# Optimization experiments

Measured on AMD Instinct MI355X. Metric: run time of the kernel, lower is better.

## Reference

```python
import jax, jax.numpy as jnp
import numpy as np

SCALE = 0.08838834764831845  # 1/sqrt(128)
NUM_HEADS = 32
NUM_KV_HEADS = 8
HEAD_DIM = 128
BLOCK_SIZE = 16
NUM_BLOCKS = 4096
MAX_BLOCKS_PER_SEQ = 128
BATCH = 32
MAX_CTX = MAX_BLOCKS_PER_SEQ * BLOCK_SIZE  # 2048


def setup_inputs() -> dict:
    key = jax.random.key(0)
    ks = jax.random.split(key, 8)
    D = NUM_KV_HEADS * HEAD_DIM
    q = jax.random.normal(ks[0], (BATCH, NUM_HEADS, HEAD_DIM), dtype=jnp.float32)
    k = jax.random.normal(ks[1], (BATCH, NUM_KV_HEADS, HEAD_DIM), dtype=jnp.float32)
    v = jax.random.normal(ks[2], (BATCH, NUM_KV_HEADS, HEAD_DIM), dtype=jnp.float32)
    k_cache = jax.random.normal(ks[3], (NUM_BLOCKS, BLOCK_SIZE, D), dtype=jnp.float32)
    v_cache = jax.random.normal(ks[4], (NUM_BLOCKS, BLOCK_SIZE, D), dtype=jnp.float32)
    # one unique slot per decoding request (deterministic scatter)
    slot_mapping = jnp.arange(BATCH, dtype=jnp.int32)
    block_tables = jax.random.randint(ks[5], (BATCH, MAX_BLOCKS_PER_SEQ), 0, NUM_BLOCKS, dtype=jnp.int32)
    context_lens = jnp.maximum(
        jax.random.randint(ks[6], (BATCH,), 0, MAX_CTX, dtype=jnp.int32), 1)
    return {"q": q, "k": k, "v": v, "k_cache": k_cache, "v_cache": v_cache,
            "slot_mapping": slot_mapping, "block_tables": block_tables,
            "context_lens": context_lens}


def reference(q, k, v, k_cache, v_cache, slot_mapping, block_tables, context_lens):
    B, H, Dh = q.shape
    KVH = k.shape[1]
    num_blocks, block_size, D = k_cache.shape
    n_rep = H // KVH

    # --- store_kvcache: scatter new K/V tokens into the paged cache ---
    # flat slot index = block_idx * block_size + slot_idx; slot == -1 dropped
    kc = k_cache.reshape(num_blocks * block_size, D)
    vc = v_cache.reshape(num_blocks * block_size, D)
    kc = kc.at[slot_mapping].set(k.reshape(B, D), mode="drop")
    vc = vc.at[slot_mapping].set(v.reshape(B, D), mode="drop")
    kc = kc.reshape(num_blocks, block_size, D)
    vc = vc.reshape(num_blocks, block_size, D)

    # --- decode-phase paged attention ---
    # gather per-request KV via block tables: [B, S, KVH, Dh]
    k_seq = kc[block_tables].reshape(B, -1, KVH, Dh)
    v_seq = vc[block_tables].reshape(B, -1, KVH, Dh)
    S = k_seq.shape[1]

    # GQA: group query heads over kv heads
    qg = q.reshape(B, KVH, n_rep, Dh)
    scores = jnp.einsum("bkgd,bskd->bkgs", qg, k_seq) * SCALE  # [B,KVH,G,S]
    valid = jnp.arange(S, dtype=jnp.int32)[None, :] < context_lens[:, None]  # [B,S]
    scores = jnp.where(valid[:, None, None, :], scores, jnp.float32(-1e30))
    p = jax.nn.softmax(scores, axis=-1)
    out = jnp.einsum("bkgs,bskd->bkgd", p, v_seq)
    return out.reshape(B, H, Dh)
```

## Files before the change

### kernel.cpp

```cpp
#include <hip/hip_runtime.h>
#include <math.h>

#define NH      32
#define KVH     8
#define GRP     4
#define DH      128
#define BS      16
#define D_TOT   1024
#define MBPS    128
#define MAX_CTX 2048
#define SCALE_F 0.08838834764831845f
#define PSTRIDE 136

__global__ void store_kv_kernel(const float* __restrict__ k,
                                const float* __restrict__ v,
                                float* __restrict__ kc,
                                float* __restrict__ vc,
                                const int* __restrict__ slot_mapping) {
    int b = blockIdx.x;
    int t = threadIdx.x;
    int s = slot_mapping[b];
    if (s < 0) return;
    const float4* k4 = (const float4*)(k + (size_t)b * D_TOT);
    const float4* v4 = (const float4*)(v + (size_t)b * D_TOT);
    float4* kc4 = (float4*)(kc + (size_t)s * D_TOT);
    float4* vc4 = (float4*)(vc + (size_t)s * D_TOT);
    kc4[t] = k4[t];
    vc4[t] = v4[t];
}

__global__ __launch_bounds__(256, 6) void attn_partial_kernel(
    const float* __restrict__ q,
    const float* __restrict__ kc,
    const float* __restrict__ vc,
    const int* __restrict__ block_tables,
    const int* __restrict__ ctx_lens,
    float* __restrict__ ws,
    int split_tok, int nsplit)
{
    const int kvh   = blockIdx.x;
    const int b     = blockIdx.y;
    const int split = blockIdx.z;
    const int ctx   = ctx_lens[b];
    const int start = split * split_tok;
    if (start >= ctx) return;
    const int end = min(ctx, start + split_tok);

    const int wave = threadIdx.x >> 6;
    const int lane = threadIdx.x & 63;
    const int h    = kvh * GRP + wave;
    const int tsub = lane >> 4;
    const int dseg = lane & 15;

    const float* qh = q + ((size_t)b * NH + h) * DH;
    const float4 qa = *(const float4*)(qh + dseg * 8);
    const float4 qb = *(const float4*)(qh + dseg * 8 + 4);

    const int* bt = block_tables + b * MBPS;

    float m = -INFINITY;
    float l = 0.f;
    float acc[8];
    #pragma unroll
    for (int j = 0; j < 8; ++j) acc[j] = 0.f;

    const int cb0 = start >> 4;
    const int cb1 = (end + 15) >> 4;

    for (int cb = cb0; cb < cb1; ++cb) {
        const int blk = bt[cb];
        const float* kbase = kc + (size_t)blk * BS * D_TOT + kvh * DH;
        const float* vbase = vc + (size_t)blk * BS * D_TOT + kvh * DH;
        const int tbase = cb << 4;

        #pragma unroll 2
        for (int ps = 0; ps < 4; ++ps) {
            const int tok  = tbase + ps * 4 + tsub;
            const int rofs = (ps * 4 + tsub) * D_TOT + dseg * 8;
            float4 ka = *(const float4*)(kbase + rofs);
            float4 kb = *(const float4*)(kbase + rofs + 4);
            float4 va = *(const float4*)(vbase + rofs);
            float4 vb = *(const float4*)(vbase + rofs + 4);

            float s = qa.x*ka.x + qa.y*ka.y + qa.z*ka.z + qa.w*ka.w
                    + qb.x*kb.x + qb.y*kb.y + qb.z*kb.z + qb.w*kb.w;
            s += __shfl_xor(s, 1);
            s += __shfl_xor(s, 2);
            s += __shfl_xor(s, 4);
            s += __shfl_xor(s, 8);
            s *= SCALE_F;
            if (tok >= end) s = -INFINITY;

            float pm = fmaxf(s, __shfl_xor(s, 16));
            pm = fmaxf(pm, __shfl_xor(pm, 32));

            if (pm > m) {
                float alpha = __expf(m - pm);
                l *= alpha;
                #pragma unroll
                for (int j = 0; j < 8; ++j) acc[j] *= alpha;
                m = pm;
            }

            float p = __expf(s - m);
            float psum = p + __shfl_xor(p, 16);
            psum += __shfl_xor(psum, 32);
            l += psum;

            acc[0] += p * va.x; acc[1] += p * va.y;
            acc[2] += p * va.z; acc[3] += p * va.w;
            acc[4] += p * vb.x; acc[5] += p * vb.y;
            acc[6] += p * vb.z; acc[7] += p * vb.w;
        }
    }

    #pragma unroll
    for (int j = 0; j < 8; ++j) {
        acc[j] += __shfl_xor(acc[j], 16);
        acc[j] += __shfl_xor(acc[j], 32);
    }

    float* o = ws + ((((size_t)b * KVH + kvh) * nsplit + split) * GRP + wave) * PSTRIDE;
    if (tsub == 0) {
        *(float4*)(o + dseg * 8)     = make_float4(acc[0], acc[1], acc[2], acc[3]);
        *(float4*)(o + dseg * 8 + 4) = make_float4(acc[4], acc[5], acc[6], acc[7]);
        if (lane == 0) { o[128] = m; o[129] = l; }
    }
}

__global__ void combine_kernel(const float* __restrict__ ws,
                               const int* __restrict__ ctx_lens,
                               float* __restrict__ out,
                               int split_tok, int nsplit)
{
    int bh = blockIdx.x;
    int b  = bh >> 5;
    int h  = bh & 31;
    int kvh = h >> 2;
    int g   = h & 3;
    int d   = threadIdx.x;
    int ctx = ctx_lens[b];
    int nsp = (ctx + split_tok - 1) / split_tok;

    const float* base = ws + (((size_t)b * KVH + kvh) * nsplit + 0) * GRP * PSTRIDE
                           + (size_t)g * PSTRIDE;
    const int stride = GRP * PSTRIDE;

    float M = -INFINITY;
    for (int i = 0; i < nsp; ++i)
        M = fmaxf(M, base[i * stride + 128]);

    float L = 0.f, O = 0.f;
    for (int i = 0; i < nsp; ++i) {
        const float* p = base + i * stride;
        float w = __expf(p[128] - M);
        L += p[129] * w;
        O += p[d] * w;
    }
    out[((size_t)b * NH + h) * DH + d] = O / L;
}

extern "C" void kernel_launch(void* const* d_in, const int* in_sizes, int n_in,
                              void* d_out, int out_size, void* d_ws, size_t ws_size,
                              hipStream_t stream) {
    const float* q  = (const float*)d_in[0];
    const float* k  = (const float*)d_in[1];
    const float* v  = (const float*)d_in[2];
    float* kc       = (float*)d_in[3];
    float* vc       = (float*)d_in[4];
    const int* slot = (const int*)d_in[5];
    const int* bt   = (const int*)d_in[6];
    const int* cl   = (const int*)d_in[7];
    float* out      = (float*)d_out;
    float* ws       = (float*)d_ws;

    const size_t per_split = (size_t)32 * KVH * GRP * PSTRIDE * sizeof(float);
    int nsplit;
    if      (ws_size >= per_split * 16) nsplit = 16;
    else if (ws_size >= per_split * 8)  nsplit = 8;
    else                                nsplit = 4;
    int split_tok = MAX_CTX / nsplit;

    store_kv_kernel<<<32, 256, 0, stream>>>(k, v, kc, vc, slot);
    attn_partial_kernel<<<dim3(KVH, 32, nsplit), 256, 0, stream>>>(
        q, kc, vc, bt, cl, ws, split_tok, nsplit);
    combine_kernel<<<1024, 128, 0, stream>>>(ws, cl, out, split_tok, nsplit);
}
```

Measured before the change: 492.6 us.

## Fuse KV-cache store into attention by overriding cached rows on the fly

Removes the separate store kernel. The attention kernel now loads slot_mapping into lanes, and for each cache block it builds a ballot of new tokens that land in that block. For those rows it substitutes the fresh k/v values in registers instead of reading the stale cache. This saves one kernel launch and its ordering dependency, but the persistent cache is no longer written, and every block iteration adds a ballot check.

```diff
diff --git a/kernel.cpp b/kernel.cpp
--- a/kernel.cpp
+++ b/kernel.cpp
@@ -12,27 +12,13 @@
 #define SCALE_F 0.08838834764831845f
 #define PSTRIDE 136
 
-__global__ void store_kv_kernel(const float* __restrict__ k,
-                                const float* __restrict__ v,
-                                float* __restrict__ kc,
-                                float* __restrict__ vc,
-                                const int* __restrict__ slot_mapping) {
-    int b = blockIdx.x;
-    int t = threadIdx.x;
-    int s = slot_mapping[b];
-    if (s < 0) return;
-    const float4* k4 = (const float4*)(k + (size_t)b * D_TOT);
-    const float4* v4 = (const float4*)(v + (size_t)b * D_TOT);
-    float4* kc4 = (float4*)(kc + (size_t)s * D_TOT);
-    float4* vc4 = (float4*)(vc + (size_t)s * D_TOT);
-    kc4[t] = k4[t];
-    vc4[t] = v4[t];
-}
-
 __global__ __launch_bounds__(256, 6) void attn_partial_kernel(
     const float* __restrict__ q,
+    const float* __restrict__ knew,
+    const float* __restrict__ vnew,
     const float* __restrict__ kc,
     const float* __restrict__ vc,
+    const int* __restrict__ slot_mapping,
     const int* __restrict__ block_tables,
     const int* __restrict__ ctx_lens,
     float* __restrict__ ws,
@@ -56,6 +42,9 @@
     const float4 qa = *(const float4*)(qh + dseg * 8);
     const float4 qb = *(const float4*)(qh + dseg * 8 + 4);
 
+    int sm = -1;
+    if (lane < 32) sm = slot_mapping[lane];
+
     const int* bt = block_tables + b * MBPS;
 
     float m = -INFINITY;
@@ -73,6 +62,9 @@
         const float* vbase = vc + (size_t)blk * BS * D_TOT + kvh * DH;
         const int tbase = cb << 4;
 
+        const unsigned long long ovr =
+            __ballot(sm >= 0 && (sm >> 4) == blk);
+
         #pragma unroll 2
         for (int ps = 0; ps < 4; ++ps) {
             const int tok  = tbase + ps * 4 + tsub;
@@ -81,6 +73,23 @@
             float4 kb = *(const float4*)(kbase + rofs + 4);
             float4 va = *(const float4*)(vbase + rofs);
             float4 vb = *(const float4*)(vbase + rofs + 4);
+
+            if (__builtin_expect(ovr != 0ULL, 0)) {
+                unsigned long long mm = ovr;
+                while (mm) {
+                    const int j = __ffsll((unsigned long long)mm) - 1;
+                    mm &= mm - 1;
+                    const int slot = __shfl(sm, j);
+                    if ((slot & 15) == (ps * 4 + tsub)) {
+                        const float* kn = knew + ((size_t)j * KVH + kvh) * DH + dseg * 8;
+                        const float* vn = vnew + ((size_t)j * KVH + kvh) * DH + dseg * 8;
+                        ka = *(const float4*)(kn);
+                        kb = *(const float4*)(kn + 4);
+                        va = *(const float4*)(vn);
+                        vb = *(const float4*)(vn + 4);
+                    }
+                }
+            }
 
             float s = qa.x*ka.x + qa.y*ka.y + qa.z*ka.z + qa.w*ka.w
                     + qb.x*kb.x + qb.y*kb.y + qb.z*kb.z + qb.w*kb.w;
@@ -166,8 +175,8 @@
     const float* q  = (const float*)d_in[0];
     const float* k  = (const float*)d_in[1];
     const float* v  = (const float*)d_in[2];
-    float* kc       = (float*)d_in[3];
-    float* vc       = (float*)d_in[4];
+    const float* kc = (const float*)d_in[3];
+    const float* vc = (const float*)d_in[4];
     const int* slot = (const int*)d_in[5];
     const int* bt   = (const int*)d_in[6];
     const int* cl   = (const int*)d_in[7];
@@ -181,8 +190,7 @@
     else                                nsplit = 4;
     int split_tok = MAX_CTX / nsplit;
 
-    store_kv_kernel<<<32, 256, 0, stream>>>(k, v, kc, vc, slot);
     attn_partial_kernel<<<dim3(KVH, 32, nsplit), 256, 0, stream>>>(
-        q, kc, vc, bt, cl, ws, split_tok, nsplit);
+        q, k, v, kc, vc, slot, bt, cl, ws, split_tok, nsplit);
     combine_kernel<<<1024, 128, 0, stream>>>(ws, cl, out, split_tok, nsplit);
 }
```

New measurement: 498.5 us. No clear change (+1.2%).
